# Kernel optimization log

Hardware: AMD Instinct MI355X
Metric: run time of the kernel (lower is better)

Reference implementation:

```python
import jax, jax.numpy as jnp
import numpy as np

E = 8          # num_experts
TOP_K = 2
CAP_RATIO = 1.2


def setup_inputs() -> dict:
    key = jax.random.key(0)
    k1, k2, k3, k4 = jax.random.split(key, 4)
    B, L, D, H = 2, 2048, 768, 2048
    x = jax.random.normal(k1, (B, L, D), dtype=jnp.float32)
    Wg = jax.random.normal(k2, (D, E), dtype=jnp.float32) * 0.02   # gate: Linear(D, E, bias=False)
    W1 = jax.random.normal(k3, (E, D, 2 * H), dtype=jnp.float32) * 0.02  # fc1 per expert (y | gate halves)
    W2 = jax.random.normal(k4, (E, H, D), dtype=jnp.float32) * 0.02      # fc2 per expert
    return {"x": x, "Wg": Wg, "W1": W1, "W2": W2}


def reference(x, Wg, W1, W2):
    B, L, D = x.shape
    H = W2.shape[1]
    xf = x.reshape(-1, D)                      # [N, D]
    N = xf.shape[0]
    capacity = int(CAP_RATIO * N / E)          # static, matches torch int()

    logits = xf @ Wg                           # [N, E]
    scores, idx = jax.lax.top_k(logits, TOP_K) # [N, K] (descending, like torch.topk)
    weights = jax.nn.softmax(scores, axis=-1)  # [N, K]

    # padded token table: row N is a zero token used for unfilled capacity slots
    xpad = jnp.concatenate([xf, jnp.zeros((1, D), xf.dtype)], axis=0)
    wpad_zero = jnp.zeros((1,), weights.dtype)
    out = jnp.zeros((N, D), x.dtype)

    for k in range(TOP_K):
        ik = idx[:, k]                                         # [N] expert id per token
        onehot = (ik[:, None] == jnp.arange(E)[None, :])       # [N, E]
        pos = jnp.cumsum(onehot, axis=0) - 1                   # rank within expert, ascending token order
        posk = jnp.take_along_axis(pos, ik[:, None], axis=1)[:, 0]  # [N]
        keep = posk < capacity                                 # first-come capacity (== indices[:capacity])

        # dispatch buffer [E, C]: token index per slot, N (pad) where unfilled/dropped
        buf = jnp.full((E, capacity), N, dtype=jnp.int32)
        buf = buf.at[ik, posk].set(jnp.arange(N, dtype=jnp.int32), mode="drop")

        xg = xpad[buf]                                         # [E, C, D]
        h = jnp.einsum("ecd,edh->ech", xg, W1)                 # [E, C, 2H]
        act = h[..., :H] * jax.nn.silu(h[..., H:])             # GatedMLP: y * silu(gate)
        ye = jnp.einsum("ech,ehd->ecd", act, W2)               # [E, C, D]

        wk = jnp.where(keep, weights[:, k], 0.0)               # [N]
        w_buf = jnp.concatenate([wk, wpad_zero])[buf]          # [E, C], 0 on pad slots
        out = out.at[buf.reshape(-1)].add(
            (w_buf[..., None] * ye).reshape(E * capacity, D), mode="drop"
        )

    return out.reshape(B, L, D)
```

## Files before the change

kernel.cpp:

```cpp
#include <hip/hip_runtime.h>


typedef _Float16 half8 __attribute__((ext_vector_type(8)));
typedef _Float16 half4t __attribute__((ext_vector_type(4)));
typedef float f4 __attribute__((ext_vector_type(4)));

#define N_TOK 4096
#define DDIM  768
#define HDIM  2048
#define NEXP  8
#define CAP   614
#define CAPP  640

#define XH_OFF    0L
#define W1T_OFF   6292992L
#define YB_OFF    6292992L
#define W2T_OFF   56624640L
#define ACT_OFF   81790464L
#define EIDX_OFF  123733504L
#define WTS_OFF   123766272L
#define TOKL_OFF  123799040L
#define CNT_OFF   123840000L
#define INV_OFF   123840256L

__device__ __forceinline__ void gld16(const void* g, void* l) {
  __builtin_amdgcn_global_load_lds(
      (const __attribute__((address_space(1))) unsigned int*)g,
      (__attribute__((address_space(3))) unsigned int*)l, 16, 0, 0);
}

__device__ __forceinline__ void cvt2_tile(const float* __restrict__ src,
                                          _Float16* __restrict__ dst,
                                          int R, int C, int e, int r0, int c0,
                                          float* __restrict__ tile) {
  long sb = (long)e * R * C;
  int t = threadIdx.x;
  int rrow = t >> 4, c4 = (t & 15) * 4;
#pragma unroll
  for (int h = 0; h < 2; h++)
#pragma unroll
    for (int i = 0; i < 4; i++) {
      int row = i * 16 + rrow;
      f4 v = *(const f4*)(src + sb + (long)(r0 + row) * C + c0 + h * 64 + c4);
      *(f4*)(&tile[h * 4416 + row * 69 + c4]) = v;
    }
  __syncthreads();
#pragma unroll
  for (int h = 0; h < 2; h++)
#pragma unroll
    for (int s = 0; s < 2; s++) {
      int idx = t + s * 256;
      int c = idx >> 3, ch = idx & 7;
      half8 hv;
#pragma unroll
      for (int j = 0; j < 8; j++) hv[j] = (_Float16)tile[h * 4416 + (ch * 8 + j) * 69 + c];
      *(half8*)(dst + sb + (long)(c0 + h * 64 + c) * R + r0 + ch * 8) = hv;
    }
}

__global__ __launch_bounds__(256) void prep1_kernel(const float* __restrict__ W1,
                                                    const float* __restrict__ x,
                                                    const float* __restrict__ Wg,
                                                    _Float16* __restrict__ w1t,
                                                    _Float16* __restrict__ xh,
                                                    int* __restrict__ eidx,
                                                    float* __restrict__ wts) {
  __shared__ float smem[2 * 4416];
  int b = blockIdx.x;

  if (b < 3072) {
    int e = b / 384, rem = b % 384;
    int cx = rem % 12, cy = rem / 12;
    cvt2_tile(W1, w1t, 768, 4096, e, cx * 64, cy * 128, smem);
    return;
  }

  int rb = b - 3072;
  int t = threadIdx.x;
  for (int i = t; i < DDIM * NEXP; i += 256) smem[(i & 7) * DDIM + (i >> 3)] = Wg[i];
  __syncthreads();
  int w = t >> 6, lane = t & 63;
  int tok = rb * 4 + w;
  if (tok > N_TOK) return;
  if (tok == N_TOK) {
    half4t zz; zz[0] = zz[1] = zz[2] = zz[3] = (_Float16)0.f;
#pragma unroll
    for (int j = 0; j < 3; j++) *(half4t*)(xh + (long)N_TOK * DDIM + (lane + j * 64) * 4) = zz;
    return;
  }
  const float* xr = x + (long)tok * DDIM;
#pragma unroll
  for (int j = 0; j < 3; j++) {
    f4 v = *(const f4*)(xr + (lane + j * 64) * 4);
    half4t hv;
    hv[0] = (_Float16)v[0]; hv[1] = (_Float16)v[1];
    hv[2] = (_Float16)v[2]; hv[3] = (_Float16)v[3];
    *(half4t*)(xh + (long)tok * DDIM + (lane + j * 64) * 4) = hv;
  }
  float acc[8] = {0.f, 0.f, 0.f, 0.f, 0.f, 0.f, 0.f, 0.f};
#pragma unroll
  for (int i = 0; i < 12; i++) {
    float xv = xr[i * 64 + lane];
#pragma unroll
    for (int e2 = 0; e2 < 8; e2++) acc[e2] += xv * smem[e2 * DDIM + i * 64 + lane];
  }
#pragma unroll
  for (int e2 = 0; e2 < 8; e2++) {
    float v = acc[e2];
    v += __shfl_xor(v, 32); v += __shfl_xor(v, 16); v += __shfl_xor(v, 8);
    v += __shfl_xor(v, 4);  v += __shfl_xor(v, 2);  v += __shfl_xor(v, 1);
    acc[e2] = v;
  }
  if (lane == 0) {
    float m0 = -1e30f; int i0 = 0;
#pragma unroll
    for (int e2 = 0; e2 < 8; e2++) if (acc[e2] > m0) { m0 = acc[e2]; i0 = e2; }
    float m1 = -1e30f; int i1 = 0;
#pragma unroll
    for (int e2 = 0; e2 < 8; e2++) if (e2 != i0 && acc[e2] > m1) { m1 = acc[e2]; i1 = e2; }
    float tt = __expf(m1 - m0);
    float w0 = 1.f / (1.f + tt);
    eidx[tok * 2 + 0] = i0; eidx[tok * 2 + 1] = i1;
    wts[tok * 2 + 0] = w0;  wts[tok * 2 + 1] = 1.f - w0;
  }
}

__global__ __launch_bounds__(64) void scan_kernel(const int* __restrict__ eidx,
                                                  int* __restrict__ toklist,
                                                  int* __restrict__ counts,
                                                  int* __restrict__ inv) {
  int z = blockIdx.x;
  int k = z >> 3, e = z & 7;
  int lane = threadIdx.x;
  int mye[64];
#pragma unroll
  for (int c = 0; c < 64; c++) mye[c] = eidx[(c * 64 + lane) * 2 + k];
  int base = 0;
#pragma unroll 4
  for (int c = 0; c < 64; c++) {
    int n = c * 64 + lane;
    bool pred = (mye[c] == e);
    unsigned long long mask = __ballot(pred);
    if (pred) {
      int pos = base + __popcll(mask & ((1ull << lane) - 1ull));
      if (pos < CAP) {
        toklist[z * CAPP + pos] = n;
        inv[n * 2 + k] = z * CAPP + pos;
      } else {
        inv[n * 2 + k] = -1;
      }
    }
    base += __popcll(mask);
  }
  if (lane == 0) counts[z] = (base < CAP) ? base : CAP;
}

__global__ __launch_bounds__(256, 2) void gemm1_kernel(const _Float16* __restrict__ xh,
                                                       const _Float16* __restrict__ w1t,
                                                       const float* __restrict__ W2,
                                                       _Float16* __restrict__ w2t,
                                                       const int* __restrict__ toklist,
                                                       const int* __restrict__ counts,
                                                       _Float16* __restrict__ act) {
  __shared__ char smem[49664];

  int i = blockIdx.x;
  if (i >= 1280) {
    int b2 = i - 1280;
    int e = b2 / 192, rem = b2 % 192;
    int cx = rem % 32, cy = rem / 32;
    cvt2_tile(W2, w2t, 2048, 768, e, cx * 64, cy * 128, (float*)smem);
    return;
  }

  _Float16* As = (_Float16*)smem;
  _Float16* Bs = (_Float16*)(smem + 16384);
  int* toks = (int*)(smem + 49152);

  int xcd = i & 7, j = i >> 3;
  int m = j % 5, ii = j / 5;
  int k = ii & 1, n = ii >> 1;
  int e = xcd, z = k * 8 + e;
  int count = counts[z];
  int m0 = m * 128;
  if (m0 >= count) return;
  int n0 = n * 128;

  int t = threadIdx.x;
  if (t < 128) {
    int r = m0 + t;
    toks[t] = (r < count) ? toklist[z * CAPP + r] : N_TOK;
  }
  __syncthreads();

  int lane = t & 63, w = t >> 6;
  int l8 = lane >> 3, u8 = lane & 7;

  const _Float16* ag[4]; _Float16* al[4];
#pragma unroll
  for (int s = 0; s < 4; s++) {
    int row = w * 32 + s * 8 + l8;
    ag[s] = xh + (long)toks[row] * DDIM + ((u8 ^ (row & 7)) * 8);
    al[s] = As + row * 64 + u8 * 8;
  }
  const _Float16* bg[8]; _Float16* bl[8];
#pragma unroll
  for (int s = 0; s < 8; s++) {
    int rb = w * 64 + s * 8 + l8;
    int gr = (rb < 128) ? (n0 + rb) : (2048 + n0 + (rb - 128));
    bg[s] = w1t + ((long)e * 4096 + gr) * DDIM + ((u8 ^ (rb & 7)) * 8);
    bl[s] = Bs + rb * 64 + u8 * 8;
  }

  int q = lane >> 4, m16 = lane & 15;
  int wm = w & 1, wn = w >> 1;

  f4 zero4 = {0.f, 0.f, 0.f, 0.f};
  f4 acc[4][4][2];
#pragma unroll
  for (int rt = 0; rt < 4; rt++)
#pragma unroll
    for (int ct = 0; ct < 4; ct++) { acc[rt][ct][0] = zero4; acc[rt][ct][1] = zero4; }

  for (int kk = 0; kk < DDIM; kk += 64) {
    __syncthreads();
#pragma unroll
    for (int s = 0; s < 4; s++) { gld16(ag[s], al[s]); ag[s] += 64; }
#pragma unroll
    for (int s = 0; s < 8; s++) { gld16(bg[s], bl[s]); bg[s] += 64; }
    __syncthreads();

#pragma unroll
    for (int c = 0; c < 2; c++) {
      half8 af[4], bf[4][2];
#pragma unroll
      for (int rt = 0; rt < 4; rt++) {
        int row = wm * 64 + rt * 16 + m16;
        af[rt] = *(const half8*)(As + row * 64 + (((c * 4 + q) ^ (row & 7)) * 8));
      }
#pragma unroll
      for (int ct = 0; ct < 4; ct++) {
        int cb = wn * 64 + ct * 16 + m16;
        int ph = ((c * 4 + q) ^ (cb & 7)) * 8;
        bf[ct][0] = *(const half8*)(Bs + cb * 64 + ph);
        bf[ct][1] = *(const half8*)(Bs + (128 + cb) * 64 + ph);
      }
#pragma unroll
      for (int rt = 0; rt < 4; rt++)
#pragma unroll
        for (int ct = 0; ct < 4; ct++) {
          acc[rt][ct][0] = __builtin_amdgcn_mfma_f32_16x16x32_f16(af[rt], bf[ct][0], acc[rt][ct][0], 0, 0, 0);
          acc[rt][ct][1] = __builtin_amdgcn_mfma_f32_16x16x32_f16(af[rt], bf[ct][1], acc[rt][ct][1], 0, 0, 0);
        }
    }
  }

  long ab = (long)z * CAPP * HDIM;
#pragma unroll
  for (int rt = 0; rt < 4; rt++)
#pragma unroll
    for (int ct = 0; ct < 4; ct++)
#pragma unroll
      for (int r = 0; r < 4; r++) {
        int row = m0 + wm * 64 + rt * 16 + q * 4 + r;
        int col = n0 + wn * 64 + ct * 16 + m16;
        float h1 = acc[rt][ct][0][r], h2 = acc[rt][ct][1][r];
        float s = h2 / (1.f + __expf(-h2));
        act[ab + (long)row * HDIM + col] = (_Float16)(h1 * s);
      }
}

__global__ __launch_bounds__(256, 3) void gemm2_kernel(const _Float16* __restrict__ act,
                                                       const _Float16* __restrict__ w2t,
                                                       const int* __restrict__ counts,
                                                       float* __restrict__ ybuf) {
  int i = blockIdx.x;
  int xcd = i & 7, j = i >> 3;
  int m = j % 5, t2 = j / 5;
  int k = t2 & 1, n = t2 >> 1;
  int e = xcd, z = k * 8 + e;
  int count = counts[z];
  int m0 = m * 128;
  if (m0 >= count) return;
  int n0 = n * 128;

  __shared__ _Float16 As[128 * 64];
  __shared__ _Float16 Bs[128 * 64];

  int t = threadIdx.x;
  int lane = t & 63, w = t >> 6;
  int l8 = lane >> 3, u8 = lane & 7;

  const _Float16* ag[4]; _Float16* al[4];
#pragma unroll
  for (int s = 0; s < 4; s++) {
    int row = w * 32 + s * 8 + l8;
    ag[s] = act + ((long)z * CAPP + m0 + row) * HDIM + ((u8 ^ (row & 7)) * 8);
    al[s] = As + row * 64 + u8 * 8;
  }
  const _Float16* bg[4]; _Float16* bl[4];
#pragma unroll
  for (int s = 0; s < 4; s++) {
    int rb = w * 32 + s * 8 + l8;
    bg[s] = w2t + ((long)e * DDIM + n0 + rb) * HDIM + ((u8 ^ (rb & 7)) * 8);
    bl[s] = Bs + rb * 64 + u8 * 8;
  }

  int q = lane >> 4, m16 = lane & 15;
  int wm = w & 1, wn = w >> 1;

  f4 zero4 = {0.f, 0.f, 0.f, 0.f};
  f4 acc[4][4];
#pragma unroll
  for (int rt = 0; rt < 4; rt++)
#pragma unroll
    for (int ct = 0; ct < 4; ct++) acc[rt][ct] = zero4;

  for (int kk = 0; kk < HDIM; kk += 64) {
    __syncthreads();
#pragma unroll
    for (int s = 0; s < 4; s++) { gld16(ag[s], al[s]); ag[s] += 64; }
#pragma unroll
    for (int s = 0; s < 4; s++) { gld16(bg[s], bl[s]); bg[s] += 64; }
    __syncthreads();

#pragma unroll
    for (int c = 0; c < 2; c++) {
      half8 af[4], bf[4];
#pragma unroll
      for (int rt = 0; rt < 4; rt++) {
        int row = wm * 64 + rt * 16 + m16;
        af[rt] = *(const half8*)(As + row * 64 + (((c * 4 + q) ^ (row & 7)) * 8));
      }
#pragma unroll
      for (int ct = 0; ct < 4; ct++) {
        int cb = wn * 64 + ct * 16 + m16;
        bf[ct] = *(const half8*)(Bs + cb * 64 + (((c * 4 + q) ^ (cb & 7)) * 8));
      }
#pragma unroll
      for (int rt = 0; rt < 4; rt++)
#pragma unroll
        for (int ct = 0; ct < 4; ct++)
          acc[rt][ct] = __builtin_amdgcn_mfma_f32_16x16x32_f16(af[rt], bf[ct], acc[rt][ct], 0, 0, 0);
    }
  }

#pragma unroll
  for (int rt = 0; rt < 4; rt++)
#pragma unroll
    for (int ct = 0; ct < 4; ct++)
#pragma unroll
      for (int r = 0; r < 4; r++) {
        int lr = wm * 64 + rt * 16 + q * 4 + r;
        int col = n0 + wn * 64 + ct * 16 + m16;
        ybuf[((long)z * CAPP + m0 + lr) * DDIM + col] = acc[rt][ct][r];
      }
}

__global__ __launch_bounds__(256) void gather_kernel(const float* __restrict__ ybuf,
                                                     const int* __restrict__ inv,
                                                     const float* __restrict__ wts,
                                                     float* __restrict__ out) {
  int t = threadIdx.x;
  int w = t >> 6, lane = t & 63;
  int tok = blockIdx.x * 4 + w;
  int s0 = inv[tok * 2 + 0], s1 = inv[tok * 2 + 1];
  float w0 = wts[tok * 2 + 0], w1 = wts[tok * 2 + 1];
  float acc[12];
#pragma unroll
  for (int j = 0; j < 12; j++) acc[j] = 0.f;
  int b = lane * 12;
  if (s0 >= 0) {
    const float* y = ybuf + (long)s0 * DDIM + b;
#pragma unroll
    for (int v = 0; v < 3; v++) {
      f4 qv = *(const f4*)(y + v * 4);
#pragma unroll
      for (int j = 0; j < 4; j++) acc[v * 4 + j] += w0 * qv[j];
    }
  }
  if (s1 >= 0) {
    const float* y = ybuf + (long)s1 * DDIM + b;
#pragma unroll
    for (int v = 0; v < 3; v++) {
      f4 qv = *(const f4*)(y + v * 4);
#pragma unroll
      for (int j = 0; j < 4; j++) acc[v * 4 + j] += w1 * qv[j];
    }
  }
  float* o = out + (long)tok * DDIM + b;
#pragma unroll
  for (int v = 0; v < 3; v++) {
    f4 qv;
#pragma unroll
    for (int j = 0; j < 4; j++) qv[j] = acc[v * 4 + j];
    *(f4*)(o + v * 4) = qv;
  }
}


extern "C" void kernel_launch(void* const* d_in, const int* in_sizes, int n_in,
                              void* d_out, int out_size, void* d_ws, size_t ws_size,
                              hipStream_t stream) {
  const float* x  = (const float*)d_in[0];
  const float* Wg = (const float*)d_in[1];
  const float* W1 = (const float*)d_in[2];
  const float* W2 = (const float*)d_in[3];
  float* out = (float*)d_out;
  char* ws = (char*)d_ws;

  _Float16* xh   = (_Float16*)(ws + XH_OFF);
  _Float16* w1t  = (_Float16*)(ws + W1T_OFF);
  float*    ybuf = (float*)(ws + YB_OFF);
  _Float16* w2t  = (_Float16*)(ws + W2T_OFF);
  _Float16* actb = (_Float16*)(ws + ACT_OFF);
  int* eidx      = (int*)(ws + EIDX_OFF);
  float* wts     = (float*)(ws + WTS_OFF);
  int* toklist   = (int*)(ws + TOKL_OFF);
  int* counts    = (int*)(ws + CNT_OFF);
  int* inv       = (int*)(ws + INV_OFF);

  prep1_kernel<<<4097, 256, 0, stream>>>(W1, x, Wg, w1t, xh, eidx, wts);
  scan_kernel<<<16, 64, 0, stream>>>(eidx, toklist, counts, inv);
  gemm1_kernel<<<2816, 256, 0, stream>>>(xh, w1t, W2, w2t, toklist, counts, actb);
  gemm2_kernel<<<480, 256, 0, stream>>>(actb, w2t, counts, ybuf);
  gather_kernel<<<1024, 256, 0, stream>>>(ybuf, inv, wts, out);
}
```

Before: 331.3 us.

## Overlap routing scan with W1 conversion by regrouping kernel launches

```diff
diff --git a/kernel.cpp b/kernel.cpp
--- a/kernel.cpp
+++ b/kernel.cpp
@@ -58,29 +58,17 @@
     }
 }
 
-__global__ __launch_bounds__(256) void prep1_kernel(const float* __restrict__ W1,
-                                                    const float* __restrict__ x,
-                                                    const float* __restrict__ Wg,
-                                                    _Float16* __restrict__ w1t,
-                                                    _Float16* __restrict__ xh,
-                                                    int* __restrict__ eidx,
-                                                    float* __restrict__ wts) {
-  __shared__ float smem[2 * 4416];
-  int b = blockIdx.x;
-
-  if (b < 3072) {
-    int e = b / 384, rem = b % 384;
-    int cx = rem % 12, cy = rem / 12;
-    cvt2_tile(W1, w1t, 768, 4096, e, cx * 64, cy * 128, smem);
-    return;
-  }
-
-  int rb = b - 3072;
+__global__ __launch_bounds__(256) void router_kernel(const float* __restrict__ x,
+                                                     const float* __restrict__ Wg,
+                                                     _Float16* __restrict__ xh,
+                                                     int* __restrict__ eidx,
+                                                     float* __restrict__ wts) {
+  __shared__ float wgT[NEXP * DDIM];
   int t = threadIdx.x;
-  for (int i = t; i < DDIM * NEXP; i += 256) smem[(i & 7) * DDIM + (i >> 3)] = Wg[i];
+  for (int i = t; i < DDIM * NEXP; i += 256) wgT[(i & 7) * DDIM + (i >> 3)] = Wg[i];
   __syncthreads();
   int w = t >> 6, lane = t & 63;
-  int tok = rb * 4 + w;
+  int tok = blockIdx.x * 4 + w;
   if (tok > N_TOK) return;
   if (tok == N_TOK) {
     half4t zz; zz[0] = zz[1] = zz[2] = zz[3] = (_Float16)0.f;
@@ -102,7 +90,7 @@
   for (int i = 0; i < 12; i++) {
     float xv = xr[i * 64 + lane];
 #pragma unroll
-    for (int e2 = 0; e2 < 8; e2++) acc[e2] += xv * smem[e2 * DDIM + i * 64 + lane];
+    for (int e2 = 0; e2 < 8; e2++) acc[e2] += xv * wgT[e2 * DDIM + i * 64 + lane];
   }
 #pragma unroll
   for (int e2 = 0; e2 < 8; e2++) {
@@ -125,34 +113,50 @@
   }
 }
 
-__global__ __launch_bounds__(64) void scan_kernel(const int* __restrict__ eidx,
-                                                  int* __restrict__ toklist,
-                                                  int* __restrict__ counts,
-                                                  int* __restrict__ inv) {
-  int z = blockIdx.x;
-  int k = z >> 3, e = z & 7;
-  int lane = threadIdx.x;
-  int mye[64];
-#pragma unroll
-  for (int c = 0; c < 64; c++) mye[c] = eidx[(c * 64 + lane) * 2 + k];
-  int base = 0;
-#pragma unroll 4
-  for (int c = 0; c < 64; c++) {
-    int n = c * 64 + lane;
-    bool pred = (mye[c] == e);
-    unsigned long long mask = __ballot(pred);
-    if (pred) {
-      int pos = base + __popcll(mask & ((1ull << lane) - 1ull));
-      if (pos < CAP) {
-        toklist[z * CAPP + pos] = n;
-        inv[n * 2 + k] = z * CAPP + pos;
-      } else {
-        inv[n * 2 + k] = -1;
-      }
-    }
-    base += __popcll(mask);
-  }
-  if (lane == 0) counts[z] = (base < CAP) ? base : CAP;
+__global__ __launch_bounds__(256) void scanCvt_kernel(const int* __restrict__ eidx,
+                                                      const float* __restrict__ W1,
+                                                      int* __restrict__ toklist,
+                                                      int* __restrict__ counts,
+                                                      int* __restrict__ inv,
+                                                      _Float16* __restrict__ w1t) {
+  __shared__ float smem[2 * 4416];
+  int b = blockIdx.x;
+
+  if (b < 16) {
+    if (threadIdx.x >= 64) return;
+    int z = b;
+    int k = z >> 3, e = z & 7;
+    int lane = threadIdx.x;
+    int pre[8];
+#pragma unroll
+    for (int c = 0; c < 8; c++) pre[c] = eidx[(c * 64 + lane) * 2 + k];
+    int base = 0;
+#pragma unroll
+    for (int c = 0; c < 64; c++) {
+      int my = pre[c & 7];
+      if (c < 56) pre[c & 7] = eidx[((c + 8) * 64 + lane) * 2 + k];
+      int n = c * 64 + lane;
+      bool pred = (my == e);
+      unsigned long long mask = __ballot(pred);
+      if (pred) {
+        int pos = base + __popcll(mask & ((1ull << lane) - 1ull));
+        if (pos < CAP) {
+          toklist[z * CAPP + pos] = n;
+          inv[n * 2 + k] = z * CAPP + pos;
+        } else {
+          inv[n * 2 + k] = -1;
+        }
+      }
+      base += __popcll(mask);
+    }
+    if (lane == 0) counts[z] = (base < CAP) ? base : CAP;
+    return;
+  }
+
+  int b2 = b - 16;
+  int e = b2 / 384, rem = b2 % 384;
+  int cx = rem % 12, cy = rem / 12;
+  cvt2_tile(W1, w1t, 768, 4096, e, cx * 64, cy * 128, smem);
 }
 
 __global__ __launch_bounds__(256, 2) void gemm1_kernel(const _Float16* __restrict__ xh,
@@ -420,8 +424,8 @@
   int* counts    = (int*)(ws + CNT_OFF);
   int* inv       = (int*)(ws + INV_OFF);
 
-  prep1_kernel<<<4097, 256, 0, stream>>>(W1, x, Wg, w1t, xh, eidx, wts);
-  scan_kernel<<<16, 64, 0, stream>>>(eidx, toklist, counts, inv);
+  router_kernel<<<1025, 256, 0, stream>>>(x, Wg, xh, eidx, wts);
+  scanCvt_kernel<<<3088, 256, 0, stream>>>(eidx, W1, toklist, counts, inv, w1t);
   gemm1_kernel<<<2816, 256, 0, stream>>>(xh, w1t, W2, w2t, toklist, counts, actb);
   gemm2_kernel<<<480, 256, 0, stream>>>(actb, w2t, counts, ybuf);
   gather_kernel<<<1024, 256, 0, stream>>>(ybuf, inv, wts, out);
```

Result: faster. 315.4 us (-4.8%).
